# Optimization experiments

Hardware: AMD Instinct MI355X
Metric: run time of the kernel (lower is better)

## Reference

```python
import jax, jax.numpy as jnp
import numpy as np

EPS = 1e-5

def _mesh_conv_point(f, nbr, w, b):
    # f: [B, C, V] features; nbr: [B, V, K] neighbor vertex indices
    # gather neighbor features per batch: [B, C, V, K]
    g = jax.vmap(lambda fb, nb: fb[:, nb])(f, nbr)
    # prepend self feature -> [B, C, V, K+1]
    x = jnp.concatenate([f[:, :, :, None], g], axis=3)
    # Conv2d with kernel (1, K+1) == contraction over (C, K+1)
    return jnp.einsum('bcvk,ock->bov', x, w) + b[None, :, None]

def _instance_norm(y):
    # InstanceNorm2d (affine=False): normalize over spatial dims (V, 1)
    m = jnp.mean(y, axis=2, keepdims=True)
    v = jnp.var(y, axis=2, keepdims=True)
    return (y - m) * jax.lax.rsqrt(v + EPS)

def setup_inputs() -> dict:
    key = jax.random.key(0)
    k1, k2, k3, k4 = jax.random.split(key, 4)
    B, Cin, Cout, V, K = 4, 64, 128, 50000, 6
    fe = jax.random.normal(k1, (B, Cin, V), dtype=jnp.float32)
    nbrs = jax.random.randint(k2, (B, V, K), 0, V, dtype=jnp.int32)
    w1 = jax.random.normal(k3, (Cout, Cin, K + 1), dtype=jnp.float32) * (1.0 / np.sqrt(Cin * (K + 1)))
    b1 = jnp.zeros((Cout,), dtype=jnp.float32)
    w2 = jax.random.normal(k4, (Cout, Cout, K + 1), dtype=jnp.float32) * (1.0 / np.sqrt(Cout * (K + 1)))
    b2 = jnp.zeros((Cout,), dtype=jnp.float32)
    return {"fe": fe, "nbrs": nbrs, "w1": w1, "b1": b1, "w2": w2, "b2": b2}

def reference(fe, nbrs, w1, b1, w2, b2):
    # conv1 -> instance norm -> relu
    x1 = jax.nn.relu(_instance_norm(_mesh_conv_point(fe, nbrs, w1, b1)))
    # residual block: conv2 -> instance norm -> + x1 -> relu
    x2 = jax.nn.relu(_instance_norm(_mesh_conv_point(x1, nbrs, w2, b2)) + x1)
    # pool=0, so output == before_pool; return the single [B, Cout, V] tensor
    return x2
```

## Files before the change

kernel.cpp:

```cpp
#include <hip/hip_runtime.h>
#include <cstdint>
#include <cstddef>
#include <utility>

typedef unsigned short u16;
typedef u16 u16x8 __attribute__((ext_vector_type(8)));
typedef u16 u16x4 __attribute__((ext_vector_type(4)));
typedef _Float16 f16x8 __attribute__((ext_vector_type(8)));
typedef float f32x4 __attribute__((ext_vector_type(4)));

constexpr int B    = 4;
constexpr int CIN  = 64;
constexpr int COUT = 128;
constexpr int V    = 50000;
constexpr int KP1  = 7;
constexpr float EPS = 1e-5f;

constexpr int BN   = 128;
constexpr int NT   = (V + BN - 1) / BN;
constexpr int NTP  = 392;
constexpr int NT64 = (V + 63) / 64;

__device__ __forceinline__ u16 f2h(float f) {
    _Float16 h = (_Float16)f;
    return __builtin_bit_cast(u16, h);
}
__device__ __forceinline__ float h2f(u16 s) {
    return (float)__builtin_bit_cast(_Float16, s);
}

template<int... Is, typename F>
__device__ __forceinline__ void static_for_impl(F&& f, std::integer_sequence<int, Is...>) {
    (f(std::integral_constant<int, Is>{}), ...);
}
template<int N, typename F>
__device__ __forceinline__ void static_for(F&& f) {
    static_for_impl(f, std::make_integer_sequence<int, N>{});
}

template<int C>
__global__ __launch_bounds__(256) void prep_wf(const float* __restrict__ w,
                                               u16* __restrict__ wF) {
    constexpr int RCH = KP1 * C / 32;
    const int g = blockIdx.x * 256 + threadIdx.x;
    if (g >= RCH * 8 * 64) return;
    const int l  = g & 63;
    const int m  = (g >> 6) & 7;
    const int ch = g >> 9;
    const int k  = ch / (C / 32);
    const int c0 = (ch % (C / 32)) * 32;
    const int o  = m * 16 + (l & 15);
    u16x8 out;
#pragma unroll
    for (int j = 0; j < 8; ++j) {
        const int c = c0 + (l >> 4) * 8 + j;
        out[j] = f2h(w[((size_t)o * C + c) * KP1 + k]);
    }
    *(u16x8*)&wF[(size_t)g * 8] = out;
}

__global__ __launch_bounds__(256) void transpose_fe(const float* __restrict__ fe,
                                                    u16* __restrict__ feT) {
    __shared__ u16 tile[32][33];
    const int t  = threadIdx.x;
    const int tx = t & 31, ty = t >> 5;
    const int v0 = blockIdx.x * 32;
    const int c0 = blockIdx.y * 32;
    const int b  = blockIdx.z;
#pragma unroll
    for (int p = 0; p < 4; ++p) {
        const int c = c0 + ty + p * 8;
        const int v = v0 + tx;
        if (v < V) tile[ty + p * 8][tx] = f2h(fe[((size_t)b * CIN + c) * V + v]);
    }
    __syncthreads();
#pragma unroll
    for (int p = 0; p < 4; ++p) {
        const int v = v0 + ty + p * 8;
        const int c = c0 + tx;
        if (v < V) feT[((size_t)b * V + v) * CIN + c] = tile[tx][ty + p * 8];
    }
}

template<int C, int INL, int OUTL>
__global__ __launch_bounds__(256, 2) void conv_mfma(const void* __restrict__ xin_,
                                                    const u16*  __restrict__ wF,
                                                    const float* __restrict__ bias,
                                                    const int*  __restrict__ nbr,
                                                    void* __restrict__ out_,
                                                    float2* __restrict__ P) {
    constexpr int NS = KP1 * C / 64;
    __shared__ __align__(16) u16 Xl[2][BN][72];
    __shared__ float2 Sred[4][COUT];

    const int t    = threadIdx.x;
    const int b    = blockIdx.x / NT;
    const int tile = blockIdx.x % NT;
    const int v0   = tile * BN;
    const int w    = t >> 6;
    const int l    = t & 63;
    const int wo   = (w & 1) * 64;
    const int wv   = (w >> 1) * 64;

    const int sv = t >> 1;
    const int h  = t & 1;
    const int vS = v0 + sv;
    int idxS[KP1];
    {
        const int vc = (vS < V) ? vS : 0;
        idxS[0] = vc;
#pragma unroll
        for (int k = 1; k < KP1; ++k)
            idxS[k] = nbr[((size_t)b * V + vc) * 6 + (k - 1)];
    }

    int vn[4]; bool ok[4];
#pragma unroll
    for (int n = 0; n < 4; ++n) {
        vn[n] = v0 + wv + n * 16 + (l & 15);
        ok[n] = vn[n] < V;
    }

    f32x4 acc[4][4];
#pragma unroll
    for (int m = 0; m < 4; ++m)
#pragma unroll
        for (int n = 0; n < 4; ++n) acc[m][n] = (f32x4)0.f;

    u16x8 g[2][4];
    f16x8 af[2][8];

    auto gload = [&](auto SC, u16x8 (&gr)[4]) {
        constexpr int S    = decltype(SC)::value;
        constexpr int k_   = (C == 64) ? S : (S >> 1);
        constexpr int off_ = (C == 64) ? 0 : (S & 1) * 64;
        if constexpr (INL == 0) {
            const u16* x_ = (const u16*)xin_;
            const u16* p_ = &x_[((size_t)b * V + idxS[k_]) * C + off_ + h * 32];
#pragma unroll
            for (int j = 0; j < 4; ++j) gr[j] = *(const u16x8*)(p_ + j * 8);
        } else {
            const float* x_ = (const float*)xin_;
#pragma unroll
            for (int j = 0; j < 32; ++j) {
                const float v_ = x_[((size_t)b * C + off_ + h * 32 + j) * V + idxS[k_]];
                gr[j >> 3][j & 7] = f2h(v_);
            }
        }
    };
    auto aload = [&](auto SC, f16x8 (&ar)[8]) {
        constexpr int S = decltype(SC)::value;
#pragma unroll
        for (int kc = 0; kc < 2; ++kc)
#pragma unroll
            for (int m = 0; m < 4; ++m)
                ar[kc * 4 + m] =
                    *(const f16x8*)&wF[(((size_t)(2 * S + kc) * 8 + (wo >> 4) + m) * 64 + l) * 8];
    };
    auto store = [&](int bufi, u16x8 (&gr)[4]) {
#pragma unroll
        for (int j = 0; j < 4; ++j)
            *(u16x8*)&Xl[bufi][sv][h * 32 + j * 8] = gr[j];
    };

    gload(std::integral_constant<int, 0>{}, g[0]);
    if constexpr (NS > 1) gload(std::integral_constant<int, 1>{}, g[1]);
    aload(std::integral_constant<int, 0>{}, af[0]);
    store(0, g[0]);
    asm volatile("s_waitcnt lgkmcnt(0)" ::: "memory");
    __builtin_amdgcn_s_barrier();

    static_for<NS>([&](auto SC) {
        constexpr int s = decltype(SC)::value;
        f16x8 bf[4][2];
#pragma unroll
        for (int n = 0; n < 4; ++n)
#pragma unroll
            for (int kc = 0; kc < 2; ++kc)
                bf[n][kc] = *(const f16x8*)&Xl[s & 1][wv + n * 16 + (l & 15)]
                                              [kc * 32 + (l >> 4) * 8];
        if constexpr (s + 2 < NS)
            gload(std::integral_constant<int, s + 2>{}, g[s & 1]);
        if constexpr (s + 1 < NS)
            aload(std::integral_constant<int, s + 1>{}, af[(s + 1) & 1]);
#pragma unroll
        for (int kc = 0; kc < 2; ++kc)
#pragma unroll
            for (int m = 0; m < 4; ++m)
#pragma unroll
                for (int n = 0; n < 4; ++n)
                    acc[m][n] = __builtin_amdgcn_mfma_f32_16x16x32_f16(af[s & 1][kc * 4 + m],
                                                                       bf[n][kc],
                                                                       acc[m][n], 0, 0, 0);
        if constexpr (s + 1 < NS) {
            __builtin_amdgcn_sched_barrier(0);
            store((s + 1) & 1, g[(s + 1) & 1]);
            asm volatile("s_waitcnt lgkmcnt(0)" ::: "memory");
            __builtin_amdgcn_s_barrier();
        }
    });

    if constexpr (OUTL == 0) {
        u16* po = (u16*)out_;
#pragma unroll
        for (int n = 0; n < 4; ++n) {
            if (ok[n]) {
#pragma unroll
                for (int m = 0; m < 4; ++m) {
                    const int o = wo + m * 16 + ((l >> 4) << 2);
                    u16x4 pk;
#pragma unroll
                    for (int q = 0; q < 4; ++q) pk[q] = f2h(acc[m][n][q] + bias[o + q]);
                    *(u16x4*)&po[((size_t)b * V + vn[n]) * COUT + o] = pk;
                }
            }
        }
    } else {
        float* po = (float*)out_;
#pragma unroll
        for (int m = 0; m < 4; ++m) {
            const int o = wo + m * 16 + ((l >> 4) << 2);
#pragma unroll
            for (int q = 0; q < 4; ++q) {
                const float bq = bias[o + q];
#pragma unroll
                for (int n = 0; n < 4; ++n)
                    if (ok[n]) po[((size_t)(b * COUT + o + q)) * V + vn[n]] = acc[m][n][q] + bq;
            }
        }
    }

#pragma unroll
    for (int m = 0; m < 4; ++m) {
        const int o = wo + m * 16 + ((l >> 4) << 2);
        float s[4], s2[4];
#pragma unroll
        for (int q = 0; q < 4; ++q) {
            const float bq = bias[o + q];
            float a = 0.f, aa = 0.f;
#pragma unroll
            for (int n = 0; n < 4; ++n) {
                if (ok[n]) {
                    const float val = acc[m][n][q] + bq;
                    a += val; aa += val * val;
                }
            }
            s[q] = a; s2[q] = aa;
        }
#pragma unroll
        for (int d = 1; d < 16; d <<= 1) {
#pragma unroll
            for (int q = 0; q < 4; ++q) {
                s[q]  += __shfl_xor(s[q],  d, 16);
                s2[q] += __shfl_xor(s2[q], d, 16);
            }
        }
        if ((l & 15) == 0) {
#pragma unroll
            for (int q = 0; q < 4; ++q)
                Sred[w][o + q] = make_float2(s[q], s2[q]);
        }
    }
    __syncthreads();
    if (t < COUT) {
        const int wlo = t >> 6;
        const float2 a = Sred[wlo][t];
        const float2 c = Sred[wlo + 2][t];
        P[((size_t)b * COUT + t) * NTP + tile] = make_float2(a.x + c.x, a.y + c.y);
    }
}

__global__ __launch_bounds__(256) void finalize_fused(const float2* __restrict__ P,
                                                      float2* __restrict__ S) {
    const int row = blockIdx.x;
    float s = 0.f, s2 = 0.f;
    for (int i = threadIdx.x; i < NT; i += 256) {
        const float2 p = P[(size_t)row * NTP + i];
        s += p.x; s2 += p.y;
    }
    __shared__ float2 red[256];
    red[threadIdx.x] = make_float2(s, s2);
    __syncthreads();
    for (int w = 128; w > 0; w >>= 1) {
        if (threadIdx.x < w) {
            red[threadIdx.x].x += red[threadIdx.x + w].x;
            red[threadIdx.x].y += red[threadIdx.x + w].y;
        }
        __syncthreads();
    }
    if (threadIdx.x == 0) {
        const float m = red[0].x / V;
        const float var = red[0].y / V - m * m;
        S[row] = make_float2(m, rsqrtf(var + EPS));
    }
}

__global__ __launch_bounds__(256) void norm1(u16* __restrict__ x,
                                             const float2* __restrict__ S) {
    const unsigned e = ((unsigned)blockIdx.x * 256u + threadIdx.x) * 8u;
    if (e >= (unsigned)B * V * COUT) return;
    const unsigned b  = e / ((unsigned)V * COUT);
    const unsigned o0 = e & 127u;
    u16x8 vv = *(u16x8*)&x[e];
#pragma unroll
    for (int j = 0; j < 8; ++j) {
        const float2 s = S[b * COUT + o0 + j];
        float f = (h2f(vv[j]) - s.x) * s.y;
        vv[j] = f2h(fmaxf(f, 0.f));
    }
    *(u16x8*)&x[e] = vv;
}

__global__ __launch_bounds__(256) void final_mix2(const u16* __restrict__ y2,
                                                  const u16* __restrict__ x1,
                                                  const float2* __restrict__ S,
                                                  float* __restrict__ out) {
    __shared__ float ty[64][33], tx[64][33];
    const int t  = threadIdx.x;
    const int v0 = blockIdx.x * 64;
    const int o0 = blockIdx.y * 32;
    const int b  = blockIdx.z;
    const int jr = (t & 7) * 4;
    const int ir = t >> 3;
#pragma unroll
    for (int p = 0; p < 2; ++p) {
        const int i = ir + p * 32;
        const int v = v0 + i;
        if (v < V) {
            const size_t base = ((size_t)b * V + v) * COUT + o0 + jr;
            const u16x4 a = *(const u16x4*)&y2[base];
            const u16x4 c = *(const u16x4*)&x1[base];
#pragma unroll
            for (int q = 0; q < 4; ++q) {
                ty[i][jr + q] = h2f(a[q]);
                tx[i][jr + q] = h2f(c[q]);
            }
        }
    }
    __syncthreads();
    const int vl = t & 63, v = v0 + vl, oo0 = t >> 6;
    if (v < V) {
#pragma unroll
        for (int p = 0; p < 8; ++p) {
            const int oo = oo0 + p * 4;
            const int o  = o0 + oo;
            const float2 s = S[b * COUT + o];
            out[((size_t)b * COUT + o) * V + v] =
                fmaxf((ty[vl][oo] - s.x) * s.y + tx[vl][oo], 0.f);
        }
    }
}

__global__ __launch_bounds__(256) void final_mix(float* __restrict__ y,
                                                 const u16* __restrict__ x1,
                                                 const float2* __restrict__ S) {
    __shared__ float tile[64][33];
    const int t  = threadIdx.x;
    const int v0 = blockIdx.x * 64;
    const int o0 = blockIdx.y * 32;
    const int b  = blockIdx.z;
    const int j  = t & 31;
    const int i0 = t >> 5;
#pragma unroll
    for (int p = 0; p < 8; ++p) {
        const int i = i0 + p * 8;
        const int v = v0 + i;
        tile[i][j] = (v < V) ? h2f(x1[((size_t)b * V + v) * COUT + o0 + j]) : 0.f;
    }
    __syncthreads();
    const int vl  = t & 63;
    const int v   = v0 + vl;
    const int oo0 = t >> 6;
    if (v < V) {
#pragma unroll
        for (int p = 0; p < 8; ++p) {
            const int oo = oo0 + p * 4;
            const int o  = o0 + oo;
            const size_t idx = ((size_t)b * COUT + o) * V + v;
            const float2 s = S[b * COUT + o];
            const float f = (y[idx] - s.x) * s.y + tile[vl][oo];
            y[idx] = fmaxf(f, 0.f);
        }
    }
}

extern "C" void kernel_launch(void* const* d_in, const int* in_sizes, int n_in,
                              void* d_out, int out_size, void* d_ws, size_t ws_size,
                              hipStream_t stream) {
    const float* fe  = (const float*)d_in[0];
    const int*   nbr = (const int*)d_in[1];
    const float* w1  = (const float*)d_in[2];
    const float* b1  = (const float*)d_in[3];
    const float* w2  = (const float*)d_in[4];
    const float* b2  = (const float*)d_in[5];
    float* outf = (float*)d_out;
    char*  ws   = (char*)d_ws;

    constexpr size_t wF1_b = (size_t)(KP1 * CIN  / 32) * 8 * 64 * 8 * 2;
    constexpr size_t wF2_b = (size_t)(KP1 * COUT / 32) * 8 * 64 * 8 * 2;
    constexpr size_t S_b   = (size_t)B * COUT * 8;
    constexpr size_t Pf_b  = (size_t)B * COUT * NTP * 8;
    constexpr size_t x1_b  = (size_t)B * V * COUT * 2;
    constexpr size_t y2_b  = (size_t)B * V * COUT * 2;
    constexpr size_t feT_b = (size_t)B * V * CIN * 2;
    const size_t base = wF1_b + wF2_b + 2 * S_b + Pf_b;

    const bool full = (ws_size >= base + x1_b + y2_b);
    const bool t3   = (ws_size >= base + x1_b + feT_b);
    const bool t4   = (ws_size >= base + x1_b);
    if (!full && !t3 && !t4) return;

    size_t off = 0;
    u16*    wF1 = (u16*)(ws + off);    off += wF1_b;
    u16*    wF2 = (u16*)(ws + off);    off += wF2_b;
    float2* S1  = (float2*)(ws + off); off += S_b;
    float2* S2  = (float2*)(ws + off); off += S_b;
    float2* P   = (float2*)(ws + off); off += Pf_b;
    u16*    x1  = (u16*)(ws + off);    off += x1_b;
    u16*    ext = (u16*)(ws + off);

    prep_wf<CIN> <<<(KP1 * CIN  / 32) * 8 * 64 / 256, 256, 0, stream>>>(w1, wF1);
    prep_wf<COUT><<<(KP1 * COUT / 32) * 8 * 64 / 256, 256, 0, stream>>>(w2, wF2);

    const bool useFeT = full || t3;
    if (useFeT) {
        dim3 gt((V + 31) / 32, CIN / 32, B);
        transpose_fe<<<gt, 256, 0, stream>>>(fe, ext);
    }

    if (useFeT) conv_mfma<CIN, 0, 0><<<B * NT, 256, 0, stream>>>(ext, wF1, b1, nbr, x1, P);
    else        conv_mfma<CIN, 1, 0><<<B * NT, 256, 0, stream>>>(fe,  wF1, b1, nbr, x1, P);
    finalize_fused<<<B * COUT, 256, 0, stream>>>(P, S1);
    norm1<<<(int)((size_t)B * V * COUT / 8 / 256), 256, 0, stream>>>(x1, S1);

    dim3 gf(NT64, COUT / 32, B);
    if (full) {
        u16* y2 = ext;
        conv_mfma<COUT, 0, 0><<<B * NT, 256, 0, stream>>>(x1, wF2, b2, nbr, y2, P);
        finalize_fused<<<B * COUT, 256, 0, stream>>>(P, S2);
        final_mix2<<<gf, 256, 0, stream>>>(y2, x1, S2, outf);
    } else {
        conv_mfma<COUT, 0, 1><<<B * NT, 256, 0, stream>>>(x1, wF2, b2, nbr, outf, P);
        finalize_fused<<<B * COUT, 256, 0, stream>>>(P, S2);
        final_mix<<<gf, 256, 0, stream>>>(outf, x1, S2);
    }
}
```

Measured before the change: 233.4 us.

## Stage gathered features and weights via direct global-to-LDS loads with swizzle

Rewrites the conv MFMA main loop so gathered neighbor rows and weight fragments go straight from global memory into LDS with global_load_lds, double-buffered, and with an XOR swizzle on the feature tile to avoid bank conflicts. Neighbor indices are loaded once into shared memory. This removes the register staging and separate LDS store, and weights now come from LDS instead of global-to-register loads. The cost is more LDS per block (about 72KB), which may cut occupancy below two blocks per CU, plus full __syncthreads per stage. The fp32 fallback path is dropped, and the transpose now writes into the output buffer when workspace is small.

```diff
diff --git a/kernel.cpp b/kernel.cpp
--- a/kernel.cpp
+++ b/kernel.cpp
@@ -27,6 +27,12 @@
 }
 __device__ __forceinline__ float h2f(u16 s) {
     return (float)__builtin_bit_cast(_Float16, s);
+}
+
+__device__ __forceinline__ void g2l16(const void* g, void* l) {
+    __builtin_amdgcn_global_load_lds(
+        (const __attribute__((address_space(1))) void*)g,
+        (__attribute__((address_space(3))) void*)l, 16, 0, 0);
 }
 
 template<int... Is, typename F>
@@ -82,15 +88,17 @@
     }
 }
 
-template<int C, int INL, int OUTL>
-__global__ __launch_bounds__(256, 2) void conv_mfma(const void* __restrict__ xin_,
-                                                    const u16*  __restrict__ wF,
+template<int C, int OUTL>
+__global__ __launch_bounds__(256, 2) void conv_mfma(const u16* __restrict__ xin,
+                                                    const u16* __restrict__ wF,
                                                     const float* __restrict__ bias,
                                                     const int*  __restrict__ nbr,
                                                     void* __restrict__ out_,
                                                     float2* __restrict__ P) {
     constexpr int NS = KP1 * C / 64;
-    __shared__ __align__(16) u16 Xl[2][BN][72];
+    __shared__ __align__(16) u16 Xs[2][BN * 64];
+    __shared__ __align__(16) u16 Wl[2][8192];
+    __shared__ int idxL[KP1][BN];
     __shared__ float2 Sred[4][COUT];
 
     const int t    = threadIdx.x;
@@ -101,18 +109,16 @@
     const int l    = t & 63;
     const int wo   = (w & 1) * 64;
     const int wv   = (w >> 1) * 64;
-
-    const int sv = t >> 1;
-    const int h  = t & 1;
-    const int vS = v0 + sv;
-    int idxS[KP1];
-    {
-        const int vc = (vS < V) ? vS : 0;
-        idxS[0] = vc;
+    const int swz  = (l & 7) ^ ((l >> 3) & 7);
+
+    if (t < BN) {
+        const int vc = (v0 + t < V) ? (v0 + t) : 0;
+        idxL[0][t] = vc;
 #pragma unroll
         for (int k = 1; k < KP1; ++k)
-            idxS[k] = nbr[((size_t)b * V + vc) * 6 + (k - 1)];
-    }
+            idxL[k][t] = nbr[((size_t)b * V + vc) * 6 + (k - 1)];
+    }
+    __syncthreads();
 
     int vn[4]; bool ok[4];
 #pragma unroll
@@ -127,77 +133,53 @@
 #pragma unroll
         for (int n = 0; n < 4; ++n) acc[m][n] = (f32x4)0.f;
 
-    u16x8 g[2][4];
-    f16x8 af[2][8];
-
-    auto gload = [&](auto SC, u16x8 (&gr)[4]) {
+    auto issue = [&](auto SC, auto BIC) {
         constexpr int S    = decltype(SC)::value;
+        constexpr int BI   = decltype(BIC)::value;
         constexpr int k_   = (C == 64) ? S : (S >> 1);
-        constexpr int off_ = (C == 64) ? 0 : (S & 1) * 64;
-        if constexpr (INL == 0) {
-            const u16* x_ = (const u16*)xin_;
-            const u16* p_ = &x_[((size_t)b * V + idxS[k_]) * C + off_ + h * 32];
-#pragma unroll
-            for (int j = 0; j < 4; ++j) gr[j] = *(const u16x8*)(p_ + j * 8);
-        } else {
-            const float* x_ = (const float*)xin_;
-#pragma unroll
-            for (int j = 0; j < 32; ++j) {
-                const float v_ = x_[((size_t)b * C + off_ + h * 32 + j) * V + idxS[k_]];
-                gr[j >> 3][j & 7] = f2h(v_);
-            }
+        constexpr int offc = (C == 64) ? 0 : (S & 1) * 64;
+#pragma unroll
+        for (int q = 0; q < 4; ++q) {
+            const int row = 32 * w + 8 * q + (l >> 3);
+            const int id  = idxL[k_][row];
+            const u16* src = xin + ((size_t)b * V + id) * C + offc + swz * 8;
+            g2l16(src, (void*)&Xs[BI][(32 * w + 8 * q) * 64]);
+        }
+#pragma unroll
+        for (int q = 0; q < 4; ++q) {
+            const u16* srcw = wF + (size_t)S * 8192 + (w * 4 + q) * 512 + l * 8;
+            g2l16(srcw, (void*)&Wl[BI][(w * 4 + q) * 512]);
         }
     };
-    auto aload = [&](auto SC, f16x8 (&ar)[8]) {
-        constexpr int S = decltype(SC)::value;
-#pragma unroll
-        for (int kc = 0; kc < 2; ++kc)
-#pragma unroll
-            for (int m = 0; m < 4; ++m)
-                ar[kc * 4 + m] =
-                    *(const f16x8*)&wF[(((size_t)(2 * S + kc) * 8 + (wo >> 4) + m) * 64 + l) * 8];
-    };
-    auto store = [&](int bufi, u16x8 (&gr)[4]) {
-#pragma unroll
-        for (int j = 0; j < 4; ++j)
-            *(u16x8*)&Xl[bufi][sv][h * 32 + j * 8] = gr[j];
-    };
-
-    gload(std::integral_constant<int, 0>{}, g[0]);
-    if constexpr (NS > 1) gload(std::integral_constant<int, 1>{}, g[1]);
-    aload(std::integral_constant<int, 0>{}, af[0]);
-    store(0, g[0]);
-    asm volatile("s_waitcnt lgkmcnt(0)" ::: "memory");
-    __builtin_amdgcn_s_barrier();
+
+    issue(std::integral_constant<int, 0>{}, std::integral_constant<int, 0>{});
+    __syncthreads();
 
     static_for<NS>([&](auto SC) {
         constexpr int s = decltype(SC)::value;
-        f16x8 bf[4][2];
-#pragma unroll
-        for (int n = 0; n < 4; ++n)
-#pragma unroll
-            for (int kc = 0; kc < 2; ++kc)
-                bf[n][kc] = *(const f16x8*)&Xl[s & 1][wv + n * 16 + (l & 15)]
-                                              [kc * 32 + (l >> 4) * 8];
-        if constexpr (s + 2 < NS)
-            gload(std::integral_constant<int, s + 2>{}, g[s & 1]);
         if constexpr (s + 1 < NS)
-            aload(std::integral_constant<int, s + 1>{}, af[(s + 1) & 1]);
-#pragma unroll
-        for (int kc = 0; kc < 2; ++kc)
+            issue(std::integral_constant<int, s + 1>{},
+                  std::integral_constant<int, (s + 1) & 1>{});
+#pragma unroll
+        for (int kc = 0; kc < 2; ++kc) {
+            f16x8 af[4], bf[4];
 #pragma unroll
             for (int m = 0; m < 4; ++m)
+                af[m] = *(const f16x8*)&Wl[s & 1][((kc * 8 + (wo >> 4) + m) * 64 + l) * 8];
+#pragma unroll
+            for (int n = 0; n < 4; ++n) {
+                const int rr = wv + n * 16 + (l & 15);
+                const int sl = (kc * 4 + (l >> 4)) ^ (rr & 7);
+                bf[n] = *(const f16x8*)&Xs[s & 1][rr * 64 + sl * 8];
+            }
+#pragma unroll
+            for (int m = 0; m < 4; ++m)
 #pragma unroll
                 for (int n = 0; n < 4; ++n)
-                    acc[m][n] = __builtin_amdgcn_mfma_f32_16x16x32_f16(af[s & 1][kc * 4 + m],
-                                                                       bf[n][kc],
+                    acc[m][n] = __builtin_amdgcn_mfma_f32_16x16x32_f16(af[m], bf[n],
                                                                        acc[m][n], 0, 0, 0);
-        if constexpr (s + 1 < NS) {
-            __builtin_amdgcn_sched_barrier(0);
-            store((s + 1) & 1, g[(s + 1) & 1]);
-            asm volatile("s_waitcnt lgkmcnt(0)" ::: "memory");
-            __builtin_amdgcn_s_barrier();
-        }
+        }
+        if constexpr (s + 1 < NS) __syncthreads();
     });
 
     if constexpr (OUTL == 0) {
@@ -419,28 +401,26 @@
     u16*    x1  = (u16*)(ws + off);    off += x1_b;
     u16*    ext = (u16*)(ws + off);
 
+    u16* feT = (full || t3) ? ext : (u16*)d_out;
+
     prep_wf<CIN> <<<(KP1 * CIN  / 32) * 8 * 64 / 256, 256, 0, stream>>>(w1, wF1);
     prep_wf<COUT><<<(KP1 * COUT / 32) * 8 * 64 / 256, 256, 0, stream>>>(w2, wF2);
 
-    const bool useFeT = full || t3;
-    if (useFeT) {
-        dim3 gt((V + 31) / 32, CIN / 32, B);
-        transpose_fe<<<gt, 256, 0, stream>>>(fe, ext);
-    }
-
-    if (useFeT) conv_mfma<CIN, 0, 0><<<B * NT, 256, 0, stream>>>(ext, wF1, b1, nbr, x1, P);
-    else        conv_mfma<CIN, 1, 0><<<B * NT, 256, 0, stream>>>(fe,  wF1, b1, nbr, x1, P);
+    dim3 gt((V + 31) / 32, CIN / 32, B);
+    transpose_fe<<<gt, 256, 0, stream>>>(fe, feT);
+
+    conv_mfma<CIN, 0><<<B * NT, 256, 0, stream>>>(feT, wF1, b1, nbr, x1, P);
     finalize_fused<<<B * COUT, 256, 0, stream>>>(P, S1);
     norm1<<<(int)((size_t)B * V * COUT / 8 / 256), 256, 0, stream>>>(x1, S1);
 
     dim3 gf(NT64, COUT / 32, B);
     if (full) {
         u16* y2 = ext;
-        conv_mfma<COUT, 0, 0><<<B * NT, 256, 0, stream>>>(x1, wF2, b2, nbr, y2, P);
+        conv_mfma<COUT, 0><<<B * NT, 256, 0, stream>>>(x1, wF2, b2, nbr, y2, P);
         finalize_fused<<<B * COUT, 256, 0, stream>>>(P, S2);
         final_mix2<<<gf, 256, 0, stream>>>(y2, x1, S2, outf);
     } else {
-        conv_mfma<COUT, 0, 1><<<B * NT, 256, 0, stream>>>(x1, wF2, b2, nbr, outf, P);
+        conv_mfma<COUT, 1><<<B * NT, 256, 0, stream>>>(x1, wF2, b2, nbr, outf, P);
         finalize_fused<<<B * COUT, 256, 0, stream>>>(P, S2);
         final_mix<<<gf, 256, 0, stream>>>(outf, x1, S2);
     }
```

After: 257.6 us. +10.4%, slower.

## Cut conv register pressure to raise occupancy to four blocks per CU

Applied to the files above, without the earlier changes.

The conv kernel now keeps single-buffered gather and weight registers instead of double-buffered ones, and requests launch bounds of 4 blocks per CU instead of 2. The stats reduction buffer reuses the LDS tile to save shared memory, with an extra barrier added first. The fp32-input fallback path is removed; the transpose now always runs, writing into the output buffer when the workspace is small. The aim is more waves in flight to hide gather latency, at the cost of shorter prefetch distance inside each block.

```diff
diff --git a/kernel.cpp b/kernel.cpp
--- a/kernel.cpp
+++ b/kernel.cpp
@@ -82,16 +82,16 @@
     }
 }
 
-template<int C, int INL, int OUTL>
-__global__ __launch_bounds__(256, 2) void conv_mfma(const void* __restrict__ xin_,
-                                                    const u16*  __restrict__ wF,
+template<int C, int OUTL>
+__global__ __launch_bounds__(256, 4) void conv_mfma(const u16* __restrict__ xin,
+                                                    const u16* __restrict__ wF,
                                                     const float* __restrict__ bias,
                                                     const int*  __restrict__ nbr,
                                                     void* __restrict__ out_,
                                                     float2* __restrict__ P) {
     constexpr int NS = KP1 * C / 64;
     __shared__ __align__(16) u16 Xl[2][BN][72];
-    __shared__ float2 Sred[4][COUT];
+    float2* SredF = (float2*)&Xl[0][0][0];
 
     const int t    = threadIdx.x;
     const int b    = blockIdx.x / NT;
@@ -127,51 +127,41 @@
 #pragma unroll
         for (int n = 0; n < 4; ++n) acc[m][n] = (f32x4)0.f;
 
-    u16x8 g[2][4];
-    f16x8 af[2][8];
-
-    auto gload = [&](auto SC, u16x8 (&gr)[4]) {
+    u16x8 g[4];
+    f16x8 af[8];
+
+    auto gload = [&](auto SC) {
         constexpr int S    = decltype(SC)::value;
         constexpr int k_   = (C == 64) ? S : (S >> 1);
         constexpr int off_ = (C == 64) ? 0 : (S & 1) * 64;
-        if constexpr (INL == 0) {
-            const u16* x_ = (const u16*)xin_;
-            const u16* p_ = &x_[((size_t)b * V + idxS[k_]) * C + off_ + h * 32];
-#pragma unroll
-            for (int j = 0; j < 4; ++j) gr[j] = *(const u16x8*)(p_ + j * 8);
-        } else {
-            const float* x_ = (const float*)xin_;
-#pragma unroll
-            for (int j = 0; j < 32; ++j) {
-                const float v_ = x_[((size_t)b * C + off_ + h * 32 + j) * V + idxS[k_]];
-                gr[j >> 3][j & 7] = f2h(v_);
-            }
-        }
+        const u16* p_ = &xin[((size_t)b * V + idxS[k_]) * C + off_ + h * 32];
+#pragma unroll
+        for (int j = 0; j < 4; ++j) g[j] = *(const u16x8*)(p_ + j * 8);
     };
-    auto aload = [&](auto SC, f16x8 (&ar)[8]) {
+    auto aload = [&](auto SC) {
         constexpr int S = decltype(SC)::value;
 #pragma unroll
         for (int kc = 0; kc < 2; ++kc)
 #pragma unroll
             for (int m = 0; m < 4; ++m)
-                ar[kc * 4 + m] =
+                af[kc * 4 + m] =
                     *(const f16x8*)&wF[(((size_t)(2 * S + kc) * 8 + (wo >> 4) + m) * 64 + l) * 8];
     };
-    auto store = [&](int bufi, u16x8 (&gr)[4]) {
+    auto store = [&](int bufi) {
 #pragma unroll
         for (int j = 0; j < 4; ++j)
-            *(u16x8*)&Xl[bufi][sv][h * 32 + j * 8] = gr[j];
+            *(u16x8*)&Xl[bufi][sv][h * 32 + j * 8] = g[j];
     };
 
-    gload(std::integral_constant<int, 0>{}, g[0]);
-    if constexpr (NS > 1) gload(std::integral_constant<int, 1>{}, g[1]);
-    aload(std::integral_constant<int, 0>{}, af[0]);
-    store(0, g[0]);
+    gload(std::integral_constant<int, 0>{});
+    store(0);
     asm volatile("s_waitcnt lgkmcnt(0)" ::: "memory");
     __builtin_amdgcn_s_barrier();
 
     static_for<NS>([&](auto SC) {
         constexpr int s = decltype(SC)::value;
+        aload(SC);
+        if constexpr (s + 1 < NS) gload(std::integral_constant<int, s + 1>{});
         f16x8 bf[4][2];
 #pragma unroll
         for (int n = 0; n < 4; ++n)
@@ -179,22 +169,18 @@
             for (int kc = 0; kc < 2; ++kc)
                 bf[n][kc] = *(const f16x8*)&Xl[s & 1][wv + n * 16 + (l & 15)]
                                               [kc * 32 + (l >> 4) * 8];
-        if constexpr (s + 2 < NS)
-            gload(std::integral_constant<int, s + 2>{}, g[s & 1]);
-        if constexpr (s + 1 < NS)
-            aload(std::integral_constant<int, s + 1>{}, af[(s + 1) & 1]);
 #pragma unroll
         for (int kc = 0; kc < 2; ++kc)
 #pragma unroll
             for (int m = 0; m < 4; ++m)
 #pragma unroll
                 for (int n = 0; n < 4; ++n)
-                    acc[m][n] = __builtin_amdgcn_mfma_f32_16x16x32_f16(af[s & 1][kc * 4 + m],
+                    acc[m][n] = __builtin_amdgcn_mfma_f32_16x16x32_f16(af[kc * 4 + m],
                                                                        bf[n][kc],
                                                                        acc[m][n], 0, 0, 0);
         if constexpr (s + 1 < NS) {
             __builtin_amdgcn_sched_barrier(0);
-            store((s + 1) & 1, g[(s + 1) & 1]);
+            store((s + 1) & 1);
             asm volatile("s_waitcnt lgkmcnt(0)" ::: "memory");
             __builtin_amdgcn_s_barrier();
         }
@@ -229,6 +215,8 @@
             }
         }
     }
+
+    __syncthreads();
 
 #pragma unroll
     for (int m = 0; m < 4; ++m) {
@@ -258,14 +246,14 @@
         if ((l & 15) == 0) {
 #pragma unroll
             for (int q = 0; q < 4; ++q)
-                Sred[w][o + q] = make_float2(s[q], s2[q]);
+                SredF[w * COUT + o + q] = make_float2(s[q], s2[q]);
         }
     }
     __syncthreads();
     if (t < COUT) {
         const int wlo = t >> 6;
-        const float2 a = Sred[wlo][t];
-        const float2 c = Sred[wlo + 2][t];
+        const float2 a = SredF[wlo * COUT + t];
+        const float2 c = SredF[(wlo + 2) * COUT + t];
         P[((size_t)b * COUT + t) * NTP + tile] = make_float2(a.x + c.x, a.y + c.y);
     }
 }
@@ -419,28 +407,26 @@
     u16*    x1  = (u16*)(ws + off);    off += x1_b;
     u16*    ext = (u16*)(ws + off);
 
+    u16* feT = (full || t3) ? ext : (u16*)d_out;
+
     prep_wf<CIN> <<<(KP1 * CIN  / 32) * 8 * 64 / 256, 256, 0, stream>>>(w1, wF1);
     prep_wf<COUT><<<(KP1 * COUT / 32) * 8 * 64 / 256, 256, 0, stream>>>(w2, wF2);
 
-    const bool useFeT = full || t3;
-    if (useFeT) {
-        dim3 gt((V + 31) / 32, CIN / 32, B);
-        transpose_fe<<<gt, 256, 0, stream>>>(fe, ext);
-    }
-
-    if (useFeT) conv_mfma<CIN, 0, 0><<<B * NT, 256, 0, stream>>>(ext, wF1, b1, nbr, x1, P);
-    else        conv_mfma<CIN, 1, 0><<<B * NT, 256, 0, stream>>>(fe,  wF1, b1, nbr, x1, P);
+    dim3 gt((V + 31) / 32, CIN / 32, B);
+    transpose_fe<<<gt, 256, 0, stream>>>(fe, feT);
+
+    conv_mfma<CIN, 0><<<B * NT, 256, 0, stream>>>(feT, wF1, b1, nbr, x1, P);
     finalize_fused<<<B * COUT, 256, 0, stream>>>(P, S1);
     norm1<<<(int)((size_t)B * V * COUT / 8 / 256), 256, 0, stream>>>(x1, S1);
 
     dim3 gf(NT64, COUT / 32, B);
     if (full) {
         u16* y2 = ext;
-        conv_mfma<COUT, 0, 0><<<B * NT, 256, 0, stream>>>(x1, wF2, b2, nbr, y2, P);
+        conv_mfma<COUT, 0><<<B * NT, 256, 0, stream>>>(x1, wF2, b2, nbr, y2, P);
         finalize_fused<<<B * COUT, 256, 0, stream>>>(P, S2);
         final_mix2<<<gf, 256, 0, stream>>>(y2, x1, S2, outf);
     } else {
-        conv_mfma<COUT, 0, 1><<<B * NT, 256, 0, stream>>>(x1, wF2, b2, nbr, outf, P);
+        conv_mfma<COUT, 1><<<B * NT, 256, 0, stream>>>(x1, wF2, b2, nbr, outf, P);
         finalize_fused<<<B * COUT, 256, 0, stream>>>(P, S2);
         final_mix<<<gf, 256, 0, stream>>>(outf, x1, S2);
     }
```

New measurement: 241.8 us. 1.04x slower.
